# Kernel tuning notes

Hardware: AMD Instinct MI355X
Metric: run time of the kernel (lower is better)

## Reference

```python
import jax, jax.numpy as jnp
import numpy as np

EPS = 1e-5

def _h_swish(y):
    # x * relu6(x+3)/6
    return y * jnp.clip(y + 3.0, 0.0, 6.0) / 6.0

def setup_inputs() -> dict:
    key = jax.random.key(0)
    ks = jax.random.split(key, 12)
    n, c, h, w = 16, 256, 64, 64
    inp = oup = c
    mip = max(8, inp // 32)  # groups=32 -> mip=8
    return {
        "x": jax.random.normal(ks[0], (n, c, h, w), jnp.float32),
        "residual": jax.random.normal(ks[1], (n, c, h, w), jnp.float32),
        "w1": jax.random.normal(ks[2], (mip, inp), jnp.float32) * 0.05,
        "b1": jax.random.normal(ks[3], (mip,), jnp.float32) * 0.05,
        "bn_gamma": jnp.ones((mip,), jnp.float32),
        "bn_beta": jnp.zeros((mip,), jnp.float32),
        "bn_mean": jax.random.normal(ks[4], (mip,), jnp.float32) * 0.05,
        "bn_var": jax.random.uniform(ks[5], (mip,), jnp.float32, 0.5, 1.5),
        "w2": jax.random.normal(ks[6], (oup, mip), jnp.float32) * 0.05,
        "b2": jax.random.normal(ks[7], (oup,), jnp.float32) * 0.05,
        "w3": jax.random.normal(ks[8], (oup, mip), jnp.float32) * 0.05,
        "b3": jax.random.normal(ks[9], (oup,), jnp.float32) * 0.05,
    }

def reference(x, residual, w1, b1, bn_gamma, bn_beta, bn_mean, bn_var, w2, b2, w3, b3):
    n, c, h, w = x.shape
    # bilinear resize of residual to x's spatial size (align_corners=False)
    res_r = jax.image.resize(residual, x.shape, method="linear")
    xs = x + res_r  # [n,c,h,w]
    # directional average pools
    x_h = xs.mean(axis=3, keepdims=True)                      # [n,c,h,1]
    x_w = xs.mean(axis=2, keepdims=True).transpose(0, 1, 3, 2)  # [n,c,w,1]
    y = jnp.concatenate([x_h, x_w], axis=2)                   # [n,c,h+w,1]
    # 1x1 conv -> BN (inference) -> h_swish
    y = jnp.einsum("nchw,mc->nmhw", y, w1) + b1[None, :, None, None]
    inv = bn_gamma / jnp.sqrt(bn_var + EPS)
    y = (y - bn_mean[None, :, None, None]) * inv[None, :, None, None] + bn_beta[None, :, None, None]
    y = _h_swish(y)                                           # [n,mip,h+w,1]
    yh, yw = y[:, :, :h, :], y[:, :, h:, :]                   # [n,mip,h,1],[n,mip,w,1]
    yw = yw.transpose(0, 1, 3, 2)                             # [n,mip,1,w]
    a_h = jax.nn.sigmoid(jnp.einsum("nmhw,om->nohw", yh, w2) + b2[None, :, None, None])  # [n,c,h,1]
    a_w = jax.nn.sigmoid(jnp.einsum("nmhw,om->nohw", yw, w3) + b3[None, :, None, None])  # [n,c,1,w]
    wei = a_h * a_w                                           # [n,c,h,w] via broadcast
    return 2.0 * xs * wei + 2.0 * residual * (1.0 - wei)
```

## Files before the change

### kernel.cpp

```cpp
#include <hip/hip_runtime.h>
#include <math.h>

#define NB 16
#define CB 256
#define MIP 8
#define EPSV 1e-5f

__global__ __launch_bounds__(256) void k_reduce(const float* __restrict__ x,
                                                const float* __restrict__ res,
                                                float* __restrict__ xh,
                                                float* __restrict__ xw) {
    int bid = blockIdx.x;
    int plane = (bid & 7) + 8 * (511 - (bid >> 3));
    const float4* px4 = (const float4*)(x   + (size_t)plane * 4096);
    const float4* pr4 = (const float4*)(res + (size_t)plane * 4096);
    __shared__ float spad[256];
    int t = threadIdx.x;

    float4 a[4], b[4];
#pragma unroll
    for (int i = 0; i < 4; i++) a[i] = px4[i * 256 + t];
#pragma unroll
    for (int i = 0; i < 4; i++) b[i] = pr4[i * 256 + t];

    float csum0 = 0.f, csum1 = 0.f, csum2 = 0.f, csum3 = 0.f;
    float rsum[4];
#pragma unroll
    for (int i = 0; i < 4; i++) {
        float s0 = a[i].x + b[i].x, s1 = a[i].y + b[i].y;
        float s2 = a[i].z + b[i].z, s3 = a[i].w + b[i].w;
        csum0 += s0; csum1 += s1; csum2 += s2; csum3 += s3;
        rsum[i] = (s0 + s1) + (s2 + s3);
    }
#pragma unroll
    for (int i = 0; i < 4; i++) {
        float rs = rsum[i];
        rs += __shfl_xor(rs, 1);
        rs += __shfl_xor(rs, 2);
        rs += __shfl_xor(rs, 4);
        rs += __shfl_xor(rs, 8);
        rsum[i] = rs;
    }
    if ((t & 15) == 0) {
        int g = t >> 4;
#pragma unroll
        for (int i = 0; i < 4; i++)
            xh[(size_t)plane * 64 + i * 16 + g] = rsum[i] * 0.015625f;
    }
    csum0 += __shfl_xor(csum0, 16); csum0 += __shfl_xor(csum0, 32);
    csum1 += __shfl_xor(csum1, 16); csum1 += __shfl_xor(csum1, 32);
    csum2 += __shfl_xor(csum2, 16); csum2 += __shfl_xor(csum2, 32);
    csum3 += __shfl_xor(csum3, 16); csum3 += __shfl_xor(csum3, 32);
    int wv = t >> 6;
    int j  = t & 15;
    if ((t & 63) < 16) {
        float* d = &spad[wv * 64 + j * 4];
        d[0] = csum0; d[1] = csum1; d[2] = csum2; d[3] = csum3;
    }
    __syncthreads();
    if (t < 64)
        xw[(size_t)plane * 64 + t] =
            (spad[t] + spad[64 + t] + spad[128 + t] + spad[192 + t]) * 0.015625f;
}

__global__ __launch_bounds__(256) void k_mid(const float* __restrict__ xh,
                                             const float* __restrict__ xw,
                                             const float* __restrict__ w1,
                                             const float* __restrict__ b1,
                                             const float* __restrict__ gamma,
                                             const float* __restrict__ beta,
                                             const float* __restrict__ mean,
                                             const float* __restrict__ var,
                                             const float* __restrict__ w2,
                                             const float* __restrict__ b2,
                                             const float* __restrict__ w3,
                                             const float* __restrict__ b3,
                                             float* __restrict__ ah,
                                             float* __restrict__ aw) {
    int n  = blockIdx.x >> 3;
    int pc = blockIdx.x & 7;
    int t  = threadIdx.x;
    int ph = t & 15;
    int p  = pc * 16 + ph;
    int m  = (t >> 4) & 7;
    int half = t >> 7;
    __shared__ float part[256];
    __shared__ float ylds[MIP * 16];

    const float* pool = (p < 64) ? (xh + ((size_t)n * CB) * 64 + p)
                                 : (xw + ((size_t)n * CB) * 64 + (p - 64));
    float acc = 0.f;
    int c0 = half * 128;
#pragma unroll 16
    for (int ci = 0; ci < 128; ci++) {
        int c = c0 + ci;
        acc += pool[(size_t)c * 64] * w1[m * CB + c];
    }
    part[t] = acc;
    __syncthreads();
    if (t < 128) {
        float val = part[t] + part[t + 128] + b1[m];
        float inv = gamma[m] * rsqrtf(var[m] + EPSV);
        val = (val - mean[m]) * inv + beta[m];
        float cl = fminf(fmaxf(val + 3.f, 0.f), 6.f);
        ylds[m * 16 + ph] = val * cl * (1.f / 6.f);
    }
    __syncthreads();

    const float* wsel = (p < 64) ? w2 : w3;
    const float* bsel = (p < 64) ? b2 : b3;
    float* osel = (p < 64) ? (ah + ((size_t)n * CB) * 64 + p)
                           : (aw + ((size_t)n * CB) * 64 + (p - 64));
#pragma unroll
    for (int oo = 0; oo < 16; oo++) {
        int o = oo * 16 + (t >> 4);
        float acc2 = bsel[o];
#pragma unroll
        for (int mm = 0; mm < MIP; mm++)
            acc2 += wsel[o * MIP + mm] * ylds[mm * 16 + ph];
        osel[(size_t)o * 64] = 1.f / (1.f + __expf(-acc2));
    }
}

__global__ __launch_bounds__(256) void k_apply(const float* __restrict__ x,
                                               const float* __restrict__ res,
                                               const float* __restrict__ ah,
                                               const float* __restrict__ aw,
                                               float* __restrict__ out) {
    int plane = blockIdx.x;
    const float4* px4 = (const float4*)(x   + (size_t)plane * 4096);
    const float4* pr4 = (const float4*)(res + (size_t)plane * 4096);
    float4*       po4 = (float4*)(out + (size_t)plane * 4096);
    __shared__ float sah[64], saw[64];
    int t = threadIdx.x;
    if (t < 64)       sah[t]      = ah[(size_t)plane * 64 + t];
    else if (t < 128) saw[t - 64] = aw[(size_t)plane * 64 + (t - 64)];
    __syncthreads();
    const float4 sw4 = *(const float4*)&saw[4 * (t & 15)];
#pragma unroll
    for (int i = 0; i < 4; i++) {
        int row = i * 16 + (t >> 4);
        float ahr2 = 2.f * sah[row];
        float4 a = px4[i * 256 + t];
        float4 b = pr4[i * 256 + t];
        float4 oo;
        oo.x = a.x * (ahr2 * sw4.x) + 2.f * b.x;
        oo.y = a.y * (ahr2 * sw4.y) + 2.f * b.y;
        oo.z = a.z * (ahr2 * sw4.z) + 2.f * b.z;
        oo.w = a.w * (ahr2 * sw4.w) + 2.f * b.w;
        po4[i * 256 + t] = oo;
    }
}

extern "C" void kernel_launch(void* const* d_in, const int* in_sizes, int n_in,
                              void* d_out, int out_size, void* d_ws, size_t ws_size,
                              hipStream_t stream) {
    const float* x     = (const float*)d_in[0];
    const float* res   = (const float*)d_in[1];
    const float* w1    = (const float*)d_in[2];
    const float* b1    = (const float*)d_in[3];
    const float* gamma = (const float*)d_in[4];
    const float* beta  = (const float*)d_in[5];
    const float* mean  = (const float*)d_in[6];
    const float* var   = (const float*)d_in[7];
    const float* w2    = (const float*)d_in[8];
    const float* b2    = (const float*)d_in[9];
    const float* w3    = (const float*)d_in[10];
    const float* b3    = (const float*)d_in[11];
    float* out = (float*)d_out;

    float* ws = (float*)d_ws;
    float* xh = ws;
    float* xw = ws + 262144;
    float* ah = ws + 524288;
    float* aw = ws + 786432;

    k_reduce<<<NB * CB, 256, 0, stream>>>(x, res, xh, xw);
    k_mid<<<NB * 8, 256, 0, stream>>>(xh, xw, w1, b1, gamma, beta, mean, var,
                                      w2, b2, w3, b3, ah, aw);
    k_apply<<<NB * CB, 256, 0, stream>>>(x, res, ah, aw, out);
}
```

Measured before the change: 57.34 us.

## Split batch in halves and fuse second-half reduce with first-half apply

The batch is split into two halves of eight images. The pooling reduction of the second half runs in the same kernel as the apply pass of the first half, using interleaved block types. The goal is to overlap the streaming reads and writes and shrink the serial gaps around the tiny mid kernel. The cost is five launches instead of three, and the reduce and apply blocks may compete for bandwidth.

```diff
diff --git a/kernel.cpp b/kernel.cpp
--- a/kernel.cpp
+++ b/kernel.cpp
@@ -6,30 +6,26 @@
 #define MIP 8
 #define EPSV 1e-5f
 
-__global__ __launch_bounds__(256) void k_reduce(const float* __restrict__ x,
-                                                const float* __restrict__ res,
-                                                float* __restrict__ xh,
-                                                float* __restrict__ xw) {
-    int bid = blockIdx.x;
-    int plane = (bid & 7) + 8 * (511 - (bid >> 3));
+
+__device__ __forceinline__ void reduce_plane(
+    const float* __restrict__ x, const float* __restrict__ res,
+    float* __restrict__ xh, float* __restrict__ xw,
+    int plane, int t, float* spad)
+{
     const float4* px4 = (const float4*)(x   + (size_t)plane * 4096);
     const float4* pr4 = (const float4*)(res + (size_t)plane * 4096);
-    __shared__ float spad[256];
-    int t = threadIdx.x;
-
     float4 a[4], b[4];
 #pragma unroll
     for (int i = 0; i < 4; i++) a[i] = px4[i * 256 + t];
 #pragma unroll
     for (int i = 0; i < 4; i++) b[i] = pr4[i * 256 + t];
-
-    float csum0 = 0.f, csum1 = 0.f, csum2 = 0.f, csum3 = 0.f;
+    float cs0 = 0.f, cs1 = 0.f, cs2 = 0.f, cs3 = 0.f;
     float rsum[4];
 #pragma unroll
     for (int i = 0; i < 4; i++) {
         float s0 = a[i].x + b[i].x, s1 = a[i].y + b[i].y;
         float s2 = a[i].z + b[i].z, s3 = a[i].w + b[i].w;
-        csum0 += s0; csum1 += s1; csum2 += s2; csum3 += s3;
+        cs0 += s0; cs1 += s1; cs2 += s2; cs3 += s3;
         rsum[i] = (s0 + s1) + (s2 + s3);
     }
 #pragma unroll
@@ -47,15 +43,15 @@
         for (int i = 0; i < 4; i++)
             xh[(size_t)plane * 64 + i * 16 + g] = rsum[i] * 0.015625f;
     }
-    csum0 += __shfl_xor(csum0, 16); csum0 += __shfl_xor(csum0, 32);
-    csum1 += __shfl_xor(csum1, 16); csum1 += __shfl_xor(csum1, 32);
-    csum2 += __shfl_xor(csum2, 16); csum2 += __shfl_xor(csum2, 32);
-    csum3 += __shfl_xor(csum3, 16); csum3 += __shfl_xor(csum3, 32);
+    cs0 += __shfl_xor(cs0, 16); cs0 += __shfl_xor(cs0, 32);
+    cs1 += __shfl_xor(cs1, 16); cs1 += __shfl_xor(cs1, 32);
+    cs2 += __shfl_xor(cs2, 16); cs2 += __shfl_xor(cs2, 32);
+    cs3 += __shfl_xor(cs3, 16); cs3 += __shfl_xor(cs3, 32);
     int wv = t >> 6;
     int j  = t & 15;
     if ((t & 63) < 16) {
         float* d = &spad[wv * 64 + j * 4];
-        d[0] = csum0; d[1] = csum1; d[2] = csum2; d[3] = csum3;
+        d[0] = cs0; d[1] = cs1; d[2] = cs2; d[3] = cs3;
     }
     __syncthreads();
     if (t < 64)
@@ -63,76 +59,14 @@
             (spad[t] + spad[64 + t] + spad[128 + t] + spad[192 + t]) * 0.015625f;
 }
 
-__global__ __launch_bounds__(256) void k_mid(const float* __restrict__ xh,
-                                             const float* __restrict__ xw,
-                                             const float* __restrict__ w1,
-                                             const float* __restrict__ b1,
-                                             const float* __restrict__ gamma,
-                                             const float* __restrict__ beta,
-                                             const float* __restrict__ mean,
-                                             const float* __restrict__ var,
-                                             const float* __restrict__ w2,
-                                             const float* __restrict__ b2,
-                                             const float* __restrict__ w3,
-                                             const float* __restrict__ b3,
-                                             float* __restrict__ ah,
-                                             float* __restrict__ aw) {
-    int n  = blockIdx.x >> 3;
-    int pc = blockIdx.x & 7;
-    int t  = threadIdx.x;
-    int ph = t & 15;
-    int p  = pc * 16 + ph;
-    int m  = (t >> 4) & 7;
-    int half = t >> 7;
-    __shared__ float part[256];
-    __shared__ float ylds[MIP * 16];
-
-    const float* pool = (p < 64) ? (xh + ((size_t)n * CB) * 64 + p)
-                                 : (xw + ((size_t)n * CB) * 64 + (p - 64));
-    float acc = 0.f;
-    int c0 = half * 128;
-#pragma unroll 16
-    for (int ci = 0; ci < 128; ci++) {
-        int c = c0 + ci;
-        acc += pool[(size_t)c * 64] * w1[m * CB + c];
-    }
-    part[t] = acc;
-    __syncthreads();
-    if (t < 128) {
-        float val = part[t] + part[t + 128] + b1[m];
-        float inv = gamma[m] * rsqrtf(var[m] + EPSV);
-        val = (val - mean[m]) * inv + beta[m];
-        float cl = fminf(fmaxf(val + 3.f, 0.f), 6.f);
-        ylds[m * 16 + ph] = val * cl * (1.f / 6.f);
-    }
-    __syncthreads();
-
-    const float* wsel = (p < 64) ? w2 : w3;
-    const float* bsel = (p < 64) ? b2 : b3;
-    float* osel = (p < 64) ? (ah + ((size_t)n * CB) * 64 + p)
-                           : (aw + ((size_t)n * CB) * 64 + (p - 64));
-#pragma unroll
-    for (int oo = 0; oo < 16; oo++) {
-        int o = oo * 16 + (t >> 4);
-        float acc2 = bsel[o];
-#pragma unroll
-        for (int mm = 0; mm < MIP; mm++)
-            acc2 += wsel[o * MIP + mm] * ylds[mm * 16 + ph];
-        osel[(size_t)o * 64] = 1.f / (1.f + __expf(-acc2));
-    }
-}
-
-__global__ __launch_bounds__(256) void k_apply(const float* __restrict__ x,
-                                               const float* __restrict__ res,
-                                               const float* __restrict__ ah,
-                                               const float* __restrict__ aw,
-                                               float* __restrict__ out) {
-    int plane = blockIdx.x;
+__device__ __forceinline__ void apply_plane(
+    const float* __restrict__ x, const float* __restrict__ res,
+    const float* __restrict__ ah, const float* __restrict__ aw,
+    float* __restrict__ out, int plane, int t, float* sah, float* saw)
+{
     const float4* px4 = (const float4*)(x   + (size_t)plane * 4096);
     const float4* pr4 = (const float4*)(res + (size_t)plane * 4096);
     float4*       po4 = (float4*)(out + (size_t)plane * 4096);
-    __shared__ float sah[64], saw[64];
-    int t = threadIdx.x;
     if (t < 64)       sah[t]      = ah[(size_t)plane * 64 + t];
     else if (t < 128) saw[t - 64] = aw[(size_t)plane * 64 + (t - 64)];
     __syncthreads();
@@ -150,6 +84,99 @@
         oo.w = a.w * (ahr2 * sw4.w) + 2.f * b.w;
         po4[i * 256 + t] = oo;
     }
+}
+
+__global__ __launch_bounds__(256) void k_reduce_half(
+    const float* __restrict__ x, const float* __restrict__ res,
+    float* __restrict__ xh, float* __restrict__ xw, int img0)
+{
+    __shared__ float spad[256];
+    int bid = blockIdx.x;
+    int pl  = (bid & 7) + 8 * (255 - (bid >> 3));
+    reduce_plane(x, res, xh, xw, img0 * CB + pl, threadIdx.x, spad);
+}
+
+__global__ __launch_bounds__(256) void k_mid_half(
+    const float* __restrict__ xh, const float* __restrict__ xw,
+    const float* __restrict__ w1, const float* __restrict__ b1,
+    const float* __restrict__ gamma, const float* __restrict__ beta,
+    const float* __restrict__ mean, const float* __restrict__ var,
+    const float* __restrict__ w2, const float* __restrict__ b2,
+    const float* __restrict__ w3, const float* __restrict__ b3,
+    float* __restrict__ ah, float* __restrict__ aw, int img0)
+{
+    int n  = img0 + (blockIdx.x >> 3);
+    int pc = blockIdx.x & 7;
+    int t  = threadIdx.x;
+    int ph = t & 15;
+    int p  = pc * 16 + ph;
+    int m  = (t >> 4) & 7;
+    int half = t >> 7;
+    __shared__ float part[256];
+    __shared__ float ylds[MIP * 16];
+
+    const float* pool = (p < 64) ? (xh + ((size_t)n * CB) * 64 + p)
+                                 : (xw + ((size_t)n * CB) * 64 + (p - 64));
+    float acc = 0.f;
+    int c0 = half * 128;
+#pragma unroll 16
+    for (int ci = 0; ci < 128; ci++) {
+        int c = c0 + ci;
+        acc += pool[(size_t)c * 64] * w1[m * CB + c];
+    }
+    part[t] = acc;
+    __syncthreads();
+    if (t < 128) {
+        float val = part[t] + part[t + 128] + b1[m];
+        float inv = gamma[m] * rsqrtf(var[m] + EPSV);
+        val = (val - mean[m]) * inv + beta[m];
+        float cl = fminf(fmaxf(val + 3.f, 0.f), 6.f);
+        ylds[m * 16 + ph] = val * cl * (1.f / 6.f);
+    }
+    __syncthreads();
+    const float* wsel = (p < 64) ? w2 : w3;
+    const float* bsel = (p < 64) ? b2 : b3;
+    float* osel = (p < 64) ? (ah + ((size_t)n * CB) * 64 + p)
+                           : (aw + ((size_t)n * CB) * 64 + (p - 64));
+#pragma unroll
+    for (int oo = 0; oo < 16; oo++) {
+        int o = oo * 16 + (t >> 4);
+        float acc2 = bsel[o];
+#pragma unroll
+        for (int mm = 0; mm < MIP; mm++)
+            acc2 += wsel[o * MIP + mm] * ylds[mm * 16 + ph];
+        osel[(size_t)o * 64] = 1.f / (1.f + __expf(-acc2));
+    }
+}
+
+__global__ __launch_bounds__(256) void k_fused_ra(
+    const float* __restrict__ x, const float* __restrict__ res,
+    float* __restrict__ xh, float* __restrict__ xw,
+    const float* __restrict__ ah, const float* __restrict__ aw,
+    float* __restrict__ out, int img0_r, int img0_a)
+{
+    __shared__ float spad[256];
+    __shared__ float sah[64], saw[64];
+    int bid  = blockIdx.x;
+    int type = (bid >> 3) & 1;
+    int idx  = (bid & 7) + ((bid >> 4) << 3);
+    int t    = threadIdx.x;
+    if (type == 0) {
+        int pl = (idx & 7) + 8 * (255 - (idx >> 3));
+        reduce_plane(x, res, xh, xw, img0_r * CB + pl, t, spad);
+    } else {
+        apply_plane(x, res, ah, aw, out, img0_a * CB + idx, t, sah, saw);
+    }
+}
+
+__global__ __launch_bounds__(256) void k_apply_half(
+    const float* __restrict__ x, const float* __restrict__ res,
+    const float* __restrict__ ah, const float* __restrict__ aw,
+    float* __restrict__ out, int img0)
+{
+    __shared__ float sah[64], saw[64];
+    apply_plane(x, res, ah, aw, out, img0 * CB + blockIdx.x, threadIdx.x,
+                sah, saw);
 }
 
 extern "C" void kernel_launch(void* const* d_in, const int* in_sizes, int n_in,
@@ -175,8 +202,11 @@
     float* ah = ws + 524288;
     float* aw = ws + 786432;
 
-    k_reduce<<<NB * CB, 256, 0, stream>>>(x, res, xh, xw);
-    k_mid<<<NB * 8, 256, 0, stream>>>(xh, xw, w1, b1, gamma, beta, mean, var,
-                                      w2, b2, w3, b3, ah, aw);
-    k_apply<<<NB * CB, 256, 0, stream>>>(x, res, ah, aw, out);
-}
+    k_reduce_half<<<2048, 256, 0, stream>>>(x, res, xh, xw, 0);
+    k_mid_half<<<64, 256, 0, stream>>>(xh, xw, w1, b1, gamma, beta, mean, var,
+                                       w2, b2, w3, b3, ah, aw, 0);
+    k_fused_ra<<<4096, 256, 0, stream>>>(x, res, xh, xw, ah, aw, out, 8, 0);
+    k_mid_half<<<64, 256, 0, stream>>>(xh, xw, w1, b1, gamma, beta, mean, var,
+                                       w2, b2, w3, b3, ah, aw, 8);
+    k_apply_half<<<2048, 256, 0, stream>>>(x, res, ah, aw, out, 8);
+}
```

Result: slower. 67.00 us (+16.9%).
